# Kernel optimization log

Measured on AMD Instinct MI355X. Metric: run time of the kernel, lower is better.

The kernel has to match this reference:

```python
import jax, jax.numpy as jnp
import numpy as np

T, B, N, C, H = 4, 4, 1024, 512, 8
D = C // H
EPS = 1e-5
TAU = 2.0
SCALE = 0.125


def _bn(x, g, b, m, v):
    # eval-mode BatchNorm1d over channel dim C (last axis here)
    return (x - m) * jax.lax.rsqrt(v + EPS) * g + b


def _lif(x, v_th=1.0):
    # multi-step LIF over leading T axis: v += (x - v)/tau; spike = H(v - vth);
    # hard reset to 0 (detach_reset); sigmoid surrogate (alpha=4) straight-through
    def step(v, xt):
        v = v + (xt - v) / TAU
        sg = jax.nn.sigmoid(4.0 * (v - v_th))
        hard = (v >= v_th).astype(x.dtype)
        spike = sg + jax.lax.stop_gradient(hard - sg)
        v = v * (1.0 - jax.lax.stop_gradient(spike))
        return v, spike
    _, s = jax.lax.scan(step, jnp.zeros_like(x[0]), x)
    return s


def _heads(y):
    # [T,B,N,C] -> [T,B,H,N,D]
    return y.reshape(T, B, N, H, D).transpose(0, 1, 3, 2, 4)


def _forward(x, s_x, q_w, q_b, q_g, q_bt, q_m, q_v,
             k_w, k_b, k_g, k_bt, k_m, k_v,
             v_w, v_b, v_g, v_bt, v_m, v_v,
             p_w, p_b, p_g, p_bt, p_m, p_v):
    # s_x is flattened but never used in the original forward
    q = _heads(_lif(_bn(x @ q_w.T + q_b, q_g, q_bt, q_m, q_v)))
    k = _heads(_lif(_bn(x @ k_w.T + k_b, k_g, k_bt, k_m, k_v)))
    v = _heads(_bn(x @ v_w.T + v_b, v_g, v_bt, v_m, v_v))  # no v_lif in original forward
    attn = jnp.einsum('tbhnd,tbhmd->tbhnm', q, k) * SCALE
    o = jnp.einsum('tbhnm,tbhmd->tbhnd', attn, v)
    o = o.transpose(0, 1, 3, 2, 4).reshape(T, B, N, C)
    return _bn(o @ p_w.T + p_b, p_g, p_bt, p_m, p_v)


def setup_inputs() -> dict:
    key = jax.random.key(0)
    ks = jax.random.split(key, 10)
    def w(k):
        return jax.random.normal(k, (C, C), jnp.float32) * 0.02
    ones = jnp.ones((C,), jnp.float32)
    zeros = jnp.zeros((C,), jnp.float32)
    return {
        'x': jax.random.normal(ks[0], (T, B, N, C), jnp.float32),
        's_x': jax.random.normal(ks[1], (T, B, N, C), jnp.float32),
        'q_w': w(ks[2]), 'q_b': zeros,
        'q_g': jax.random.uniform(ks[6], (C,), jnp.float32, 0.5, 1.5), 'q_bt': zeros, 'q_m': zeros, 'q_v': ones,
        'k_w': w(ks[3]), 'k_b': zeros,
        'k_g': jax.random.uniform(ks[7], (C,), jnp.float32, 0.5, 1.5), 'k_bt': zeros, 'k_m': zeros, 'k_v': ones,
        'v_w': w(ks[4]), 'v_b': zeros,
        'v_g': jax.random.uniform(ks[8], (C,), jnp.float32, 0.5, 1.5), 'v_bt': zeros, 'v_m': zeros, 'v_v': ones,
        'p_w': w(ks[5]), 'p_b': zeros,
        'p_g': jax.random.uniform(ks[9], (C,), jnp.float32, 0.5, 1.5), 'p_bt': zeros, 'p_m': zeros, 'p_v': ones,
    }


def reference(x, s_x, q_w, q_b, q_g, q_bt, q_m, q_v,
              k_w, k_b, k_g, k_bt, k_m, k_v,
              v_w, v_b, v_g, v_bt, v_m, v_v,
              p_w, p_b, p_g, p_bt, p_m, p_v):
    return _forward(x, s_x, q_w, q_b, q_g, q_bt, q_m, q_v,
                    k_w, k_b, k_g, k_bt, k_m, k_v,
                    v_w, v_b, v_g, v_bt, v_m, v_v,
                    p_w, p_b, p_g, p_bt, p_m, p_v)
```

## Files before the change

### kernel.cpp

```cpp
#include <hip/hip_runtime.h>


#define T_ 4
#define B_ 4
#define N_ 1024
#define C_ 512
#define H_ 8
#define M_ (T_*B_*N_)

typedef __bf16 bf16x8 __attribute__((ext_vector_type(8)));
typedef float  floatx4 __attribute__((ext_vector_type(4)));

__device__ __forceinline__ float bf2f(unsigned short u) {
  union { unsigned int i; float f; } v; v.i = ((unsigned int)u) << 16; return v.f;
}
__device__ __forceinline__ unsigned short f2bf(float f) {
  unsigned int x = __float_as_uint(f);
  return (unsigned short)((x + 0x7fffu + ((x >> 16) & 1u)) >> 16);
}

#define GLOAD16(gaddr, ldsbase) \
  __builtin_amdgcn_global_load_lds((__attribute__((address_space(1))) void*)(gaddr), \
                                   (__attribute__((address_space(3))) void*)(ldsbase), 16, 0, 0)

struct BnParams { const float* p[20]; };
struct PrepArgs {
  const float *x, *qw, *kw, *vw, *pw;
  unsigned short *X2, *Wqk3, *Wvb, *Wpb;
  float *scl, *sft;
  BnParams bp;
};

__global__ __launch_bounds__(256) void prep_all(PrepArgs P) {
  const int bid = blockIdx.x;
  if (bid < 8192) {
    const int idx = (bid * 256 + threadIdx.x) * 4;
    const float4 v = *(const float4*)(P.x + idx);
    const int m = idx >> 9, k = idx & 511;
    const int t = m >> 12, b = (m >> 10) & 3, n = m & 1023;
    const int mp = (((b << 10) | n) << 2) | t;
    const size_t base = (size_t)mp * 1024 + k;
    float vv[4] = {v.x, v.y, v.z, v.w};
    unsigned short h[4], l[4];
#pragma unroll
    for (int j = 0; j < 4; ++j) { h[j] = f2bf(vv[j]); l[j] = f2bf(vv[j] - bf2f(h[j])); }
    *(ushort4*)(P.X2 + base) = ushort4{h[0], h[1], h[2], h[3]};
    *(ushort4*)(P.X2 + base + 512) = ushort4{l[0], l[1], l[2], l[3]};
  } else if (bid < 9216) {
    const int z = (bid - 8192) >> 8;
    const int idx = ((((bid - 8192) & 255) * 256) + threadIdx.x) * 4;
    const float* src = (z == 0) ? P.qw : (z == 1) ? P.kw : (z == 2) ? P.vw : P.pw;
    const float4 v = *(const float4*)(src + idx);
    if (z >= 2) {
      unsigned short* dst = (z == 2) ? P.Wvb : P.Wpb;
      *(ushort4*)(dst + idx) = ushort4{f2bf(v.x), f2bf(v.y), f2bf(v.z), f2bf(v.w)};
      return;
    }
    const int row = idx >> 9, k = idx & 511;
    unsigned short* dst = P.Wqk3 + (size_t)(z * 512) * 1536;
    const size_t base = (size_t)row * 1536 + k;
    float vv[4] = {v.x, v.y, v.z, v.w};
    unsigned short h[4], l[4];
#pragma unroll
    for (int j = 0; j < 4; ++j) { h[j] = f2bf(vv[j]); l[j] = f2bf(vv[j] - bf2f(h[j])); }
    ushort4 hi{h[0], h[1], h[2], h[3]};
    *(ushort4*)(dst + base) = hi;
    *(ushort4*)(dst + base + 512) = hi;
    *(ushort4*)(dst + base + 1024) = ushort4{l[0], l[1], l[2], l[3]};
  } else {
    const int o = (bid - 9216) * 256 + threadIdx.x;
    const int grp = o >> 9, ci = o & 511;
    const float s = P.bp.p[grp * 5 + 1][ci] * rsqrtf(P.bp.p[grp * 5 + 4][ci] + 1e-5f);
    P.scl[o] = s;
    P.sft[o] = (P.bp.p[grp * 5 + 0][ci] - P.bp.p[grp * 5 + 3][ci]) * s + P.bp.p[grp * 5 + 2][ci];
  }
}

struct Job2 {
  const unsigned short* A; int lda;
  const unsigned short* w; int ldb;
  int K, ldc, epi;
  const float* scl; const float* sft;
  float* out32; unsigned short* out16; unsigned short* out16b;
};

__global__ __launch_bounds__(512, 2) void gemm_bn(Job2 job, int lntile) {
  const int xcd = blockIdx.x & 7, slot = blockIdx.x >> 3;
  const int ntm1 = (1 << lntile) - 1;
  const int panel = xcd + 8 * (slot >> lntile);
  const int m0 = panel * 256;
  const int n0 = (slot & ntm1) * 256;

  const int tid = threadIdx.x;
  const int wv = tid >> 6, lane = tid & 63;
  const int wm = wv >> 1, wn = wv & 1;
  const int NT = job.K >> 5;

  __shared__ unsigned short AB[4][256 * 64];

  const int rloc = lane >> 3;
  const int ulog = (lane & 7) ^ rloc;
  const bool isA = ulog < 4;
  const unsigned short* bq[4];
#pragma unroll
  for (int q = 0; q < 4; ++q) {
    const int row = wv * 32 + q * 8 + rloc;
    bq[q] = isA ? job.A + (size_t)(m0 + row) * job.lda + ulog * 8
                : job.w + (size_t)(n0 + row) * job.ldb + (ulog - 4) * 8;
  }

#define ISSUE(T_, BUF_) do {                                                 \
    const int t_ = (T_);                                                     \
    const int off_ = isA ? ((t_ < 32 ? t_ : t_ - 32) << 5) : (t_ << 5);      \
    _Pragma("unroll")                                                        \
    for (int q = 0; q < 4; ++q)                                              \
      GLOAD16(bq[q] + off_, &AB[BUF_][(wv * 32 + q * 8) * 64]);              \
  } while (0)

  const int r15 = lane & 15;
  const int apos = (lane >> 4) ^ (lane & 7);
  const int bpos = (4 | (lane >> 4)) ^ (lane & 7);
  const int aoff = (wm * 64 + r15) * 64 + apos * 8;
  const int boff = (wn * 128 + r15) * 64 + bpos * 8;

  bf16x8 A0[4], A1[4], L0[4], L1[4], Hh[4];

#define RD_ALO(BUF_, AX, LX) do {                                            \
    const unsigned short* lb_ = &AB[BUF_][0];                                \
    _Pragma("unroll")                                                        \
    for (int i_ = 0; i_ < 4; ++i_) AX[i_] = *(const bf16x8*)(lb_ + aoff + i_ * 1024); \
    _Pragma("unroll")                                                        \
    for (int j_ = 0; j_ < 4; ++j_) LX[j_] = *(const bf16x8*)(lb_ + boff + j_ * 1024); \
  } while (0)

#define RD_HI(BUF_) do {                                                     \
    const unsigned short* lb_ = &AB[BUF_][0];                                \
    _Pragma("unroll")                                                        \
    for (int j_ = 0; j_ < 4; ++j_) Hh[j_] = *(const bf16x8*)(lb_ + boff + (4 + j_) * 1024); \
  } while (0)

#define MF_LO(AX, LX) do {                                                   \
    __builtin_amdgcn_s_setprio(1);                                           \
    _Pragma("unroll")                                                        \
    for (int i_ = 0; i_ < 4; ++i_)                                           \
    _Pragma("unroll")                                                        \
      for (int j_ = 0; j_ < 4; ++j_)                                         \
        acc[i_][j_] = __builtin_amdgcn_mfma_f32_16x16x32_bf16(AX[i_], LX[j_], acc[i_][j_], 0, 0, 0); \
    __builtin_amdgcn_s_setprio(0);                                           \
  } while (0)

#define MF_HI(AX) do {                                                       \
    __builtin_amdgcn_s_setprio(1);                                           \
    _Pragma("unroll")                                                        \
    for (int i_ = 0; i_ < 4; ++i_)                                           \
    _Pragma("unroll")                                                        \
      for (int j_ = 0; j_ < 4; ++j_)                                         \
        acc[i_][4 + j_] = __builtin_amdgcn_mfma_f32_16x16x32_bf16(AX[i_], Hh[j_], acc[i_][4 + j_], 0, 0, 0); \
    __builtin_amdgcn_s_setprio(0);                                           \
  } while (0)

#define MIDBAR(N_) do {                                                      \
    asm volatile("s_waitcnt vmcnt(" #N_ ")" ::: "memory");                   \
    __builtin_amdgcn_s_barrier();                                            \
    __builtin_amdgcn_sched_barrier(0);                                       \
  } while (0)

#define SLOT_I(KT_, BC_, BN_, AX, LX, AY, LY) do {                           \
    RD_HI(BC_); MF_LO(AX, LX);                                               \
    MIDBAR(8);                                                               \
    ISSUE((KT_) + 4, BC_);                                                   \
    RD_ALO(BN_, AY, LY); MF_HI(AX);                                          \
  } while (0)

  floatx4 acc[4][8];
#pragma unroll
  for (int i = 0; i < 4; ++i)
#pragma unroll
    for (int j = 0; j < 8; ++j) acc[i][j] = floatx4{0.f, 0.f, 0.f, 0.f};

  ISSUE(0, 0); ISSUE(1, 1); ISSUE(2, 2); ISSUE(3, 3);
  asm volatile("s_waitcnt vmcnt(12)" ::: "memory");
  __builtin_amdgcn_s_barrier();
  __builtin_amdgcn_sched_barrier(0);
  RD_ALO(0, A0, L0);

  const int NG = (NT - 4) >> 2;
  for (int g = 0; g < NG; ++g) {
    const int g4 = g << 2;
    SLOT_I(g4 + 0, 0, 1, A0, L0, A1, L1);
    SLOT_I(g4 + 1, 1, 2, A1, L1, A0, L0);
    SLOT_I(g4 + 2, 2, 3, A0, L0, A1, L1);
    SLOT_I(g4 + 3, 3, 0, A1, L1, A0, L0);
  }
  RD_HI(0); MF_LO(A0, L0); MIDBAR(8); RD_ALO(1, A1, L1); MF_HI(A0);
  RD_HI(1); MF_LO(A1, L1); MIDBAR(4); RD_ALO(2, A0, L0); MF_HI(A1);
  RD_HI(2); MF_LO(A0, L0); MIDBAR(0); RD_ALO(3, A1, L1); MF_HI(A0);
  RD_HI(3); MF_LO(A1, L1); MF_HI(A1);

  float scl[8], sft[8];
#pragma unroll
  for (int j = 0; j < 8; ++j) {
    const int c = n0 + wn * 128 + j * 16 + r15;
    scl[j] = job.scl[c];
    sft[j] = job.sft[c];
  }
  const int rbase = m0 + wm * 64 + (lane >> 4) * 4;

  if (job.epi == 2 && n0 < 512) {
    const int cb = n0 + wn * 128 + r15;
#pragma unroll
    for (int i = 0; i < 4; ++i) {
      unsigned short spk[4][8];
#pragma unroll
      for (int j = 0; j < 8; ++j) {
        float vme = 0.f;
#pragma unroll
        for (int r = 0; r < 4; ++r) {
          const float y = acc[i][j][r] * scl[j] + sft[j];
          vme += (y - vme) * 0.5f;
          const bool sp = vme >= 1.0f;
          spk[r][j] = sp ? (unsigned short)0x3F80 : (unsigned short)0;
          if (sp) vme = 0.f;
        }
      }
#pragma unroll
      for (int r = 0; r < 4; ++r) {
        unsigned short* prow = job.out16 + (size_t)(rbase + 16 * i + r) * 512 + cb;
#pragma unroll
        for (int j = 0; j < 8; ++j) prow[j * 16] = spk[r][j];
      }
    }
  } else if (job.epi == 2) {
    __syncthreads();
    unsigned short* lds = &AB[0][0];
    const int gq = lane >> 4;
#pragma unroll
    for (int i = 0; i < 4; ++i) {
      const int n_loc = wm * 16 + 4 * i + gq;
#pragma unroll
      for (int j = 0; j < 8; ++j) {
        const int c_loc = wn * 128 + j * 16 + r15;
        const int colbase = c_loc * 64 + (n_loc ^ ((c_loc & 7) << 3));
        float vme = 0.f;
#pragma unroll
        for (int r = 0; r < 4; ++r) {
          const float y = acc[i][j][r] * scl[j] + sft[j];
          vme += (y - vme) * 0.5f;
          const bool sp = vme >= 1.0f;
          lds[r * 16384 + colbase] = sp ? (unsigned short)0x3F80 : (unsigned short)0;
          if (sp) vme = 0.f;
        }
      }
    }
    __syncthreads();
    const int b = panel >> 4, n0g = (panel & 15) * 64, cb = n0 - 512;
#pragma unroll
    for (int it = 0; it < 16; ++it) {
      const int rho = wv * 128 + it * 8 + (lane >> 3);
      const int t = rho >> 8, c = rho & 255;
      const int nb = lane & 7;
      const uint4 d = *(const uint4*)&lds[t * 16384 + c * 64 + ((nb ^ (c & 7)) << 3)];
      *(uint4*)(job.out16b + (size_t)((t * 4 + b) * 512 + cb + c) * 1024 + n0g + nb * 8) = d;
    }
  } else {
#pragma unroll
    for (int i = 0; i < 4; ++i)
#pragma unroll
      for (int r = 0; r < 4; ++r) {
        unsigned short* prow = job.out16 + (size_t)(rbase + 16 * i + r) * job.ldc + n0 + wn * 128 + r15;
#pragma unroll
        for (int j = 0; j < 8; ++j) prow[j * 16] = f2bf(acc[i][j][r] * scl[j] + sft[j]);
      }
  }
}

__global__ __launch_bounds__(512, 2) void gemm_bn128(Job2 job) {
  const int xcd = blockIdx.x & 7, slot = blockIdx.x >> 3;
  const int panel = xcd + 8 * (slot >> 1);
  const int m0 = panel * 128;
  const int n0 = (slot & 1) * 256;

  const int tid = threadIdx.x;
  const int wv = tid >> 6, lane = tid & 63;
  const int wm = wv >> 2, wn = wv & 3;

  __shared__ unsigned short ABS[4][384 * 32];

  const unsigned short* src[3];
#pragma unroll
  for (int g = 0; g < 3; ++g) {
    const int row = wv * 48 + g * 16 + (lane >> 2);
    const int ulog = (lane & 3) ^ (row & 3);
    src[g] = (row < 128) ? job.A + (size_t)(m0 + row) * job.lda + ulog * 8
                         : job.w + (size_t)(n0 + row - 128) * job.ldb + ulog * 8;
  }

#define ISSUE1(T_, BUF_) do {                                                \
    const int k0_ = (T_) << 5;                                               \
    _Pragma("unroll")                                                        \
    for (int g_ = 0; g_ < 3; ++g_)                                           \
      GLOAD16(src[g_] + k0_, &ABS[BUF_][(wv * 48 + g_ * 16) * 32]);          \
  } while (0)

  const int r15 = lane & 15;
  const int uoff = ((lane >> 4) ^ (r15 & 3)) << 3;
  const int arow0 = (wm * 64 + r15) * 32 + uoff;
  const int brow0 = (128 + wn * 64 + r15) * 32 + uoff;

  bf16x8 AX[4], BX[4], AY[4], BY[4];
#define RD1(BUF_, A_, B_) do {                                               \
    const unsigned short* lb_ = &ABS[BUF_][0];                               \
    _Pragma("unroll")                                                        \
    for (int i_ = 0; i_ < 4; ++i_) A_[i_] = *(const bf16x8*)(lb_ + arow0 + i_ * 512); \
    _Pragma("unroll")                                                        \
    for (int j_ = 0; j_ < 4; ++j_) B_[j_] = *(const bf16x8*)(lb_ + brow0 + j_ * 512); \
  } while (0)

#define MF1(A_, B_) do {                                                     \
    __builtin_amdgcn_s_setprio(1);                                           \
    _Pragma("unroll")                                                        \
    for (int i_ = 0; i_ < 4; ++i_)                                           \
    _Pragma("unroll")                                                        \
      for (int j_ = 0; j_ < 4; ++j_)                                         \
        acc[i_][j_] = __builtin_amdgcn_mfma_f32_16x16x32_bf16(A_[i_], B_[j_], acc[i_][j_], 0, 0, 0); \
    __builtin_amdgcn_s_setprio(0);                                           \
  } while (0)

#define MB1(N_) do {                                                         \
    asm volatile("s_waitcnt vmcnt(" #N_ ")" ::: "memory");                   \
    __builtin_amdgcn_s_barrier();                                            \
    __builtin_amdgcn_sched_barrier(0);                                       \
  } while (0)

  floatx4 acc[4][4];
#pragma unroll
  for (int i = 0; i < 4; ++i)
#pragma unroll
    for (int j = 0; j < 4; ++j) acc[i][j] = floatx4{0.f, 0.f, 0.f, 0.f};

  ISSUE1(0, 0); ISSUE1(1, 1); ISSUE1(2, 2); ISSUE1(3, 3);
  asm volatile("s_waitcnt vmcnt(9)" ::: "memory");
  __builtin_amdgcn_s_barrier();
  __builtin_amdgcn_sched_barrier(0);
  RD1(0, AX, BX);

#pragma unroll 1
  for (int kt = 0; kt < 12; kt += 2) {
    MB1(6); ISSUE1(kt + 4, kt & 3);       RD1((kt + 1) & 3, AY, BY); MF1(AX, BX);
    MB1(6); ISSUE1(kt + 5, (kt + 1) & 3); RD1((kt + 2) & 3, AX, BX); MF1(AY, BY);
  }
  MB1(6); RD1(1, AY, BY); MF1(AX, BX);
  MB1(3); RD1(2, AX, BX); MF1(AY, BY);
  MB1(0); RD1(3, AY, BY); MF1(AX, BX);
  MF1(AY, BY);

  float scl[4], sft[4];
#pragma unroll
  for (int j = 0; j < 4; ++j) {
    const int c = n0 + wn * 64 + j * 16 + r15;
    scl[j] = job.scl[c];
    sft[j] = job.sft[c];
  }
  const int rbase = m0 + wm * 64 + (lane >> 4) * 4;

  if (job.epi == 4) {
    __syncthreads();
    unsigned short* lds = &ABS[0][0];
    const int gq = lane >> 4;
#pragma unroll
    for (int i = 0; i < 4; ++i) {
      const int n_loc = wm * 16 + 4 * i + gq;
#pragma unroll
      for (int j = 0; j < 4; ++j) {
        const int c_loc = wn * 64 + j * 16 + r15;
        const int colbase = c_loc * 32 + (n_loc ^ (((c_loc >> 2) & 3) << 3));
#pragma unroll
        for (int r = 0; r < 4; ++r)
          lds[r * 8192 + colbase] = f2bf(acc[i][j][r] * scl[j] + sft[j]);
      }
    }
    __syncthreads();
    const int b = panel >> 5, n0g = (panel & 31) * 32;
#pragma unroll
    for (int it = 0; it < 8; ++it) {
      const int rho = wv * 128 + it * 16 + (lane >> 2);
      const int t = rho >> 8, c = rho & 255;
      const int nb = lane & 3;
      const uint4 d = *(const uint4*)&lds[t * 8192 + c * 32 + ((nb ^ ((c >> 2) & 3)) << 3)];
      *(uint4*)(job.out16b + (size_t)((t * 4 + b) * 512 + n0 + c) * 1024 + n0g + nb * 8) = d;
    }
  } else {
#pragma unroll
    for (int i = 0; i < 4; ++i)
#pragma unroll
      for (int r = 0; r < 4; ++r) {
        const int mp = rbase + 16 * i + r;
        const int t = mp & 3, bn = mp >> 2;
        const int mstd = (((t << 2) | (bn >> 10)) << 10) | (bn & 1023);
        float* prow = job.out32 + (size_t)mstd * 512 + n0 + wn * 64 + r15;
#pragma unroll
        for (int j = 0; j < 4; ++j) prow[j * 16] = acc[i][j][r] * scl[j] + sft[j];
      }
  }
}

__global__ __launch_bounds__(256) void kv_gemm(const unsigned short* __restrict__ ktr,
                                               const unsigned short* __restrict__ vtr,
                                               unsigned short* __restrict__ kvt) {
  const int head = blockIdx.x;
  const int tb = head >> 3;
  const int h = head & 7;
  const int wv = threadIdx.x >> 6, lane = threadIdx.x & 63;
  const int m0 = wv * 256;
  const size_t cbase = (size_t)tb * C_ + h * 64;
  const int rsel = lane & 15, koff = (lane >> 4) * 8;

  floatx4 acc[4][4];
#pragma unroll
  for (int i = 0; i < 4; ++i)
#pragma unroll
    for (int j = 0; j < 4; ++j) acc[i][j] = floatx4{0.f, 0.f, 0.f, 0.f};

#pragma unroll
  for (int s = 0; s < 8; ++s) {
    const int m = m0 + s * 32 + koff;
    bf16x8 a[4], b[4];
#pragma unroll
    for (int dt = 0; dt < 4; ++dt)
      a[dt] = *(const bf16x8*)(ktr + (cbase + dt * 16 + rsel) * N_ + m);
#pragma unroll
    for (int et = 0; et < 4; ++et)
      b[et] = *(const bf16x8*)(vtr + (cbase + et * 16 + rsel) * N_ + m);
#pragma unroll
    for (int dt = 0; dt < 4; ++dt)
#pragma unroll
      for (int et = 0; et < 4; ++et)
        acc[dt][et] = __builtin_amdgcn_mfma_f32_16x16x32_bf16(a[dt], b[et], acc[dt][et], 0, 0, 0);
  }

  __shared__ float red[4096];
  const int dbase = (lane >> 4) * 4;
  const int e0 = lane & 15;
#pragma unroll 1
  for (int w = 0; w < 4; ++w) {
    if (wv == w) {
#pragma unroll
      for (int dt = 0; dt < 4; ++dt)
#pragma unroll
        for (int et = 0; et < 4; ++et)
#pragma unroll
          for (int r = 0; r < 4; ++r) {
            const int o = (dt * 16 + dbase + r) * 64 + et * 16 + e0;
            red[o] = (w == 0) ? acc[dt][et][r] : red[o] + acc[dt][et][r];
          }
    }
    __syncthreads();
  }
  const int d = threadIdx.x & 63;
  const int eg = threadIdx.x >> 6;
#pragma unroll
  for (int j = 0; j < 16; ++j) {
    const int e = eg * 16 + j;
    kvt[(size_t)head * 4096 + e * 64 + d] = f2bf(0.125f * red[d * 64 + e]);
  }
}

__global__ __launch_bounds__(256) void av_gemm(const unsigned short* __restrict__ qs,
                                               const unsigned short* __restrict__ kvt,
                                               unsigned short* __restrict__ obuf) {
  const int bx = blockIdx.x;
  const int tb = bx >> 4;
  const int sub = bx & 15;
  const int nt = sub >> 1;
  const int h0 = (sub & 1) * 4;
  const int t = tb >> 2, b = tb & 3;
  const int wv = threadIdx.x >> 6, lane = threadIdx.x & 63;
  const int n0 = nt * 128 + wv * 32;
  const int rsel = lane & 15, koff = (lane >> 4) * 8;

#pragma unroll 1
  for (int h = h0; h < h0 + 4; ++h) {
    floatx4 acc[2][4];
#pragma unroll
    for (int i = 0; i < 2; ++i)
#pragma unroll
      for (int j = 0; j < 4; ++j) acc[i][j] = floatx4{0.f, 0.f, 0.f, 0.f};
    const unsigned short* kvh = kvt + ((size_t)tb * 8 + h) * 4096;
#pragma unroll
    for (int s = 0; s < 2; ++s) {
      bf16x8 a[2], bv[4];
#pragma unroll
      for (int i = 0; i < 2; ++i) {
        const int n = n0 + i * 16 + rsel;
        a[i] = *(const bf16x8*)(qs + (size_t)((((b << 10) | n) << 2) | t) * 512 + h * 64 + s * 32 + koff);
      }
#pragma unroll
      for (int et = 0; et < 4; ++et)
        bv[et] = *(const bf16x8*)(kvh + (et * 16 + rsel) * 64 + s * 32 + koff);
#pragma unroll
      for (int i = 0; i < 2; ++i)
#pragma unroll
        for (int et = 0; et < 4; ++et)
          acc[i][et] = __builtin_amdgcn_mfma_f32_16x16x32_bf16(a[i], bv[et], acc[i][et], 0, 0, 0);
    }
#pragma unroll
    for (int i = 0; i < 2; ++i)
#pragma unroll
      for (int et = 0; et < 4; ++et)
#pragma unroll
        for (int r = 0; r < 4; ++r) {
          const int n = n0 + i * 16 + (lane >> 4) * 4 + r;
          obuf[(size_t)((((b << 10) | n) << 2) | t) * 512 + h * 64 + et * 16 + rsel] = f2bf(acc[i][et][r]);
        }
  }
}

extern "C" void kernel_launch(void* const* d_in, const int* in_sizes, int n_in,
                              void* d_out, int out_size, void* d_ws, size_t ws_size,
                              hipStream_t stream) {
  char* ws = (char*)d_ws;
  unsigned short* X2   = (unsigned short*)(ws + 0);
  unsigned short* Wqk3 = (unsigned short*)(ws + 33554432ull);
  unsigned short* Wvb  = (unsigned short*)(ws + 36700160ull);
  unsigned short* Wpb  = (unsigned short*)(ws + 37224448ull);
  float*          scl  = (float*)(ws + 37748736ull);
  float*          sft  = (float*)(ws + 37756928ull);
  unsigned short* qsb  = (unsigned short*)(ws + 41943040ull);
  unsigned short* ktr  = (unsigned short*)(ws + 58720256ull);
  unsigned short* vtr  = (unsigned short*)(ws + 75497472ull);
  unsigned short* kvt  = (unsigned short*)(ws + 92274688ull);
  unsigned short* ob   = (unsigned short*)(ws + 93323264ull);

  PrepArgs pa;
  pa.x  = (const float*)d_in[0];
  pa.qw = (const float*)d_in[2];
  pa.kw = (const float*)d_in[8];
  pa.vw = (const float*)d_in[14];
  pa.pw = (const float*)d_in[20];
  pa.X2 = X2; pa.Wqk3 = Wqk3; pa.Wvb = Wvb; pa.Wpb = Wpb;
  pa.scl = scl; pa.sft = sft;
  pa.bp.p[0]=(const float*)d_in[3];  pa.bp.p[1]=(const float*)d_in[4];  pa.bp.p[2]=(const float*)d_in[5];  pa.bp.p[3]=(const float*)d_in[6];  pa.bp.p[4]=(const float*)d_in[7];
  pa.bp.p[5]=(const float*)d_in[9];  pa.bp.p[6]=(const float*)d_in[10]; pa.bp.p[7]=(const float*)d_in[11]; pa.bp.p[8]=(const float*)d_in[12]; pa.bp.p[9]=(const float*)d_in[13];
  pa.bp.p[10]=(const float*)d_in[15];pa.bp.p[11]=(const float*)d_in[16];pa.bp.p[12]=(const float*)d_in[17];pa.bp.p[13]=(const float*)d_in[18];pa.bp.p[14]=(const float*)d_in[19];
  pa.bp.p[15]=(const float*)d_in[21];pa.bp.p[16]=(const float*)d_in[22];pa.bp.p[17]=(const float*)d_in[23];pa.bp.p[18]=(const float*)d_in[24];pa.bp.p[19]=(const float*)d_in[25];
  prep_all<<<dim3(9224), 256, 0, stream>>>(pa);

  Job2 jqk{X2, 1024, Wqk3, 1536, 1536, 512, 2, scl, sft, nullptr, qsb, ktr};
  gemm_bn<<<dim3(256), 512, 0, stream>>>(jqk, 2);

  Job2 jv{X2, 1024, Wvb, 512, 512, 512, 4, scl + 1024, sft + 1024, nullptr, nullptr, vtr};
  gemm_bn128<<<dim3(256), 512, 0, stream>>>(jv);

  kv_gemm<<<dim3(128), 256, 0, stream>>>(ktr, vtr, kvt);
  av_gemm<<<dim3(256), 256, 0, stream>>>(qsb, kvt, ob);

  Job2 jp{ob, 512, Wpb, 512, 512, 512, 3, scl + 1536, sft + 1536, (float*)d_out, nullptr, nullptr};
  gemm_bn128<<<dim3(256), 512, 0, stream>>>(jp);
}
```

Measured before the change: 126.6 us.

## Fuse QK and V projection GEMMs into one launch and split LDS B-fragment reads

Merges the QK projection GEMM and the V projection GEMM into a single 512-block kernel that dispatches on block index, sharing one LDS buffer. This removes a launch and the tail gap between the two kernels, and lets V blocks fill CUs left idle by the QK tail. It also splits the B-fragment LDS reads so the last two low fragments load along with the high ones, and reorders the MFMA loop to j-outer so the first MFMAs wait on fewer reads. The dead bf16 epilogue path is removed. The fused kernel uses the larger LDS footprint for all blocks, which may limit occupancy for the V blocks, and the mixed body may raise register pressure.

```diff
diff --git a/kernel.cpp b/kernel.cpp
--- a/kernel.cpp
+++ b/kernel.cpp
@@ -84,19 +84,17 @@
   float* out32; unsigned short* out16; unsigned short* out16b;
 };
 
-__global__ __launch_bounds__(512, 2) void gemm_bn(Job2 job, int lntile) {
-  const int xcd = blockIdx.x & 7, slot = blockIdx.x >> 3;
-  const int ntm1 = (1 << lntile) - 1;
-  const int panel = xcd + 8 * (slot >> lntile);
+__device__ __forceinline__ void qk_body(const Job2& job, int bx,
+                                        unsigned short (*AB)[256 * 64]) {
+  const int xcd = bx & 7, slot = bx >> 3;
+  const int panel = xcd + 8 * (slot >> 2);
   const int m0 = panel * 256;
-  const int n0 = (slot & ntm1) * 256;
+  const int n0 = (slot & 3) * 256;
 
   const int tid = threadIdx.x;
   const int wv = tid >> 6, lane = tid & 63;
   const int wm = wv >> 1, wn = wv & 1;
   const int NT = job.K >> 5;
-
-  __shared__ unsigned short AB[4][256 * 64];
 
   const int rloc = lane >> 3;
   const int ulog = (lane & 7) ^ rloc;
@@ -125,16 +123,18 @@
 
   bf16x8 A0[4], A1[4], L0[4], L1[4], Hh[4];
 
-#define RD_ALO(BUF_, AX, LX) do {                                            \
+#define RD_A_L01(BUF_, AX, LX) do {                                          \
     const unsigned short* lb_ = &AB[BUF_][0];                                \
     _Pragma("unroll")                                                        \
     for (int i_ = 0; i_ < 4; ++i_) AX[i_] = *(const bf16x8*)(lb_ + aoff + i_ * 1024); \
-    _Pragma("unroll")                                                        \
-    for (int j_ = 0; j_ < 4; ++j_) LX[j_] = *(const bf16x8*)(lb_ + boff + j_ * 1024); \
-  } while (0)
-
-#define RD_HI(BUF_) do {                                                     \
+    LX[0] = *(const bf16x8*)(lb_ + boff);                                    \
+    LX[1] = *(const bf16x8*)(lb_ + boff + 1024);                             \
+  } while (0)
+
+#define RD_L23_HI(BUF_, LX) do {                                             \
     const unsigned short* lb_ = &AB[BUF_][0];                                \
+    LX[2] = *(const bf16x8*)(lb_ + boff + 2 * 1024);                         \
+    LX[3] = *(const bf16x8*)(lb_ + boff + 3 * 1024);                         \
     _Pragma("unroll")                                                        \
     for (int j_ = 0; j_ < 4; ++j_) Hh[j_] = *(const bf16x8*)(lb_ + boff + (4 + j_) * 1024); \
   } while (0)
@@ -142,9 +142,9 @@
 #define MF_LO(AX, LX) do {                                                   \
     __builtin_amdgcn_s_setprio(1);                                           \
     _Pragma("unroll")                                                        \
-    for (int i_ = 0; i_ < 4; ++i_)                                           \
-    _Pragma("unroll")                                                        \
-      for (int j_ = 0; j_ < 4; ++j_)                                         \
+    for (int j_ = 0; j_ < 4; ++j_)                                           \
+    _Pragma("unroll")                                                        \
+      for (int i_ = 0; i_ < 4; ++i_)                                         \
         acc[i_][j_] = __builtin_amdgcn_mfma_f32_16x16x32_bf16(AX[i_], LX[j_], acc[i_][j_], 0, 0, 0); \
     __builtin_amdgcn_s_setprio(0);                                           \
   } while (0)
@@ -166,10 +166,10 @@
   } while (0)
 
 #define SLOT_I(KT_, BC_, BN_, AX, LX, AY, LY) do {                           \
-    RD_HI(BC_); MF_LO(AX, LX);                                               \
+    RD_L23_HI(BC_, LX); MF_LO(AX, LX);                                       \
     MIDBAR(8);                                                               \
     ISSUE((KT_) + 4, BC_);                                                   \
-    RD_ALO(BN_, AY, LY); MF_HI(AX);                                          \
+    RD_A_L01(BN_, AY, LY); MF_HI(AX);                                        \
   } while (0)
 
   floatx4 acc[4][8];
@@ -182,7 +182,7 @@
   asm volatile("s_waitcnt vmcnt(12)" ::: "memory");
   __builtin_amdgcn_s_barrier();
   __builtin_amdgcn_sched_barrier(0);
-  RD_ALO(0, A0, L0);
+  RD_A_L01(0, A0, L0);
 
   const int NG = (NT - 4) >> 2;
   for (int g = 0; g < NG; ++g) {
@@ -192,10 +192,10 @@
     SLOT_I(g4 + 2, 2, 3, A0, L0, A1, L1);
     SLOT_I(g4 + 3, 3, 0, A1, L1, A0, L0);
   }
-  RD_HI(0); MF_LO(A0, L0); MIDBAR(8); RD_ALO(1, A1, L1); MF_HI(A0);
-  RD_HI(1); MF_LO(A1, L1); MIDBAR(4); RD_ALO(2, A0, L0); MF_HI(A1);
-  RD_HI(2); MF_LO(A0, L0); MIDBAR(0); RD_ALO(3, A1, L1); MF_HI(A0);
-  RD_HI(3); MF_LO(A1, L1); MF_HI(A1);
+  RD_L23_HI(0, L0); MF_LO(A0, L0); MIDBAR(8); RD_A_L01(1, A1, L1); MF_HI(A0);
+  RD_L23_HI(1, L1); MF_LO(A1, L1); MIDBAR(4); RD_A_L01(2, A0, L0); MF_HI(A1);
+  RD_L23_HI(2, L0); MF_LO(A0, L0); MIDBAR(0); RD_A_L01(3, A1, L1); MF_HI(A0);
+  RD_L23_HI(3, L1); MF_LO(A1, L1); MF_HI(A1);
 
   float scl[8], sft[8];
 #pragma unroll
@@ -206,7 +206,7 @@
   }
   const int rbase = m0 + wm * 64 + (lane >> 4) * 4;
 
-  if (job.epi == 2 && n0 < 512) {
+  if (n0 < 512) {
     const int cb = n0 + wn * 128 + r15;
 #pragma unroll
     for (int i = 0; i < 4; ++i) {
@@ -230,7 +230,7 @@
         for (int j = 0; j < 8; ++j) prow[j * 16] = spk[r][j];
       }
     }
-  } else if (job.epi == 2) {
+  } else {
     __syncthreads();
     unsigned short* lds = &AB[0][0];
     const int gq = lane >> 4;
@@ -262,20 +262,12 @@
       const uint4 d = *(const uint4*)&lds[t * 16384 + c * 64 + ((nb ^ (c & 7)) << 3)];
       *(uint4*)(job.out16b + (size_t)((t * 4 + b) * 512 + cb + c) * 1024 + n0g + nb * 8) = d;
     }
-  } else {
-#pragma unroll
-    for (int i = 0; i < 4; ++i)
-#pragma unroll
-      for (int r = 0; r < 4; ++r) {
-        unsigned short* prow = job.out16 + (size_t)(rbase + 16 * i + r) * job.ldc + n0 + wn * 128 + r15;
-#pragma unroll
-        for (int j = 0; j < 8; ++j) prow[j * 16] = f2bf(acc[i][j][r] * scl[j] + sft[j]);
-      }
-  }
-}
-
-__global__ __launch_bounds__(512, 2) void gemm_bn128(Job2 job) {
-  const int xcd = blockIdx.x & 7, slot = blockIdx.x >> 3;
+  }
+}
+
+__device__ __forceinline__ void v_body(const Job2& job, int bx,
+                                       unsigned short (*ABS)[384 * 32]) {
+  const int xcd = bx & 7, slot = bx >> 3;
   const int panel = xcd + 8 * (slot >> 1);
   const int m0 = panel * 128;
   const int n0 = (slot & 1) * 256;
@@ -283,8 +275,6 @@
   const int tid = threadIdx.x;
   const int wv = tid >> 6, lane = tid & 63;
   const int wm = wv >> 2, wn = wv & 3;
-
-  __shared__ unsigned short ABS[4][384 * 32];
 
   const unsigned short* src[3];
 #pragma unroll
@@ -402,6 +392,17 @@
         for (int j = 0; j < 4; ++j) prow[j * 16] = acc[i][j][r] * scl[j] + sft[j];
       }
   }
+}
+
+__global__ __launch_bounds__(512, 2) void gemm_fused(Job2 jqk, Job2 jv) {
+  __shared__ unsigned short AB[4][256 * 64];
+  if (blockIdx.x < 256) qk_body(jqk, blockIdx.x, AB);
+  else                  v_body(jv, blockIdx.x - 256, (unsigned short (*)[384 * 32])AB);
+}
+
+__global__ __launch_bounds__(512, 2) void gemm128(Job2 job) {
+  __shared__ unsigned short ABS[4][384 * 32];
+  v_body(job, blockIdx.x, ABS);
 }
 
 __global__ __launch_bounds__(256) void kv_gemm(const unsigned short* __restrict__ ktr,
@@ -546,14 +547,12 @@
   prep_all<<<dim3(9224), 256, 0, stream>>>(pa);
 
   Job2 jqk{X2, 1024, Wqk3, 1536, 1536, 512, 2, scl, sft, nullptr, qsb, ktr};
-  gemm_bn<<<dim3(256), 512, 0, stream>>>(jqk, 2);
-
-  Job2 jv{X2, 1024, Wvb, 512, 512, 512, 4, scl + 1024, sft + 1024, nullptr, nullptr, vtr};
-  gemm_bn128<<<dim3(256), 512, 0, stream>>>(jv);
+  Job2 jv {X2, 1024, Wvb,  512,  512,  512, 4, scl + 1024, sft + 1024, nullptr, nullptr, vtr};
+  gemm_fused<<<dim3(512), 512, 0, stream>>>(jqk, jv);
 
   kv_gemm<<<dim3(128), 256, 0, stream>>>(ktr, vtr, kvt);
   av_gemm<<<dim3(256), 256, 0, stream>>>(qsb, kvt, ob);
 
   Job2 jp{ob, 512, Wpb, 512, 512, 512, 3, scl + 1536, sft + 1536, (float*)d_out, nullptr, nullptr};
-  gemm_bn128<<<dim3(256), 512, 0, stream>>>(jp);
-}
+  gemm128<<<dim3(256), 512, 0, stream>>>(jp);
+}
```

Result: faster. 122.1 us, median of 3 (-3.5%).
